# Kernel tuning notes

Hardware: AMD Instinct MI355X
Metric: run time of the kernel (lower is better)

Reference implementation:

```python
import math
import jax, jax.numpy as jnp
import numpy as np

NUM_HEADS = 8


def setup_inputs() -> dict:
    rng = jax.random.key(0)
    ks = jax.random.split(rng, 6)
    S, B, E = 2048, 4, 512
    scale = 1.0 / math.sqrt(E)  # xavier-ish init scale
    return {
        "query": jax.random.normal(ks[0], (S, B, E), jnp.float32),
        "key": jax.random.normal(ks[1], (S, B, E), jnp.float32),
        "value": jax.random.normal(ks[2], (S, B, E), jnp.float32),
        "attn_mask": jax.random.normal(ks[3], (B, S, S), jnp.float32),
        "in_proj_weight": jax.random.normal(ks[4], (3 * E, E), jnp.float32) * scale,
        "in_proj_bias": jnp.zeros((3 * E,), jnp.float32),
        "out_proj_weight": jax.random.normal(ks[5], (E, E), jnp.float32) * scale,
        "out_proj_bias": jnp.zeros((E,), jnp.float32),
    }


def reference(query, key, value, attn_mask, in_proj_weight, in_proj_bias,
              out_proj_weight, out_proj_bias):
    # Layout: [S, B, E] (batch_first=False)
    S, B, E = query.shape
    H = NUM_HEADS
    D = E // H
    w_q, w_k, w_v = jnp.split(in_proj_weight, 3, axis=0)  # each [E, E]
    b_q, b_k, b_v = jnp.split(in_proj_bias, 3)
    q = query @ w_q.T + b_q
    k = key @ w_k.T + b_k
    v = value @ w_v.T + b_v

    def to_heads(x):  # [S,B,E] -> [B,H,S,D]
        return x.reshape(S, B, H, D).transpose(1, 2, 0, 3)

    qh = to_heads(q) * (1.0 / math.sqrt(D))
    kh = to_heads(k)
    vh = to_heads(v)
    # full score matrix [B,H,S,S] with per-batch additive mask broadcast over heads
    scores = jnp.einsum('bhsd,bhtd->bhst', qh, kh) + attn_mask[:, None, :, :]
    attn = jax.nn.softmax(scores, axis=-1)
    out = jnp.einsum('bhst,bhtd->bhsd', attn, vh)
    out = out.transpose(2, 0, 1, 3).reshape(S, B, E)  # back to [S,B,E]
    return out @ out_proj_weight.T + out_proj_bias
```

## Files before the change

### kernel.cpp

```cpp
#include <hip/hip_runtime.h>


#define L2E 1.44269504088896340736f

typedef __attribute__((ext_vector_type(8))) __bf16 bf16x8;
typedef __attribute__((ext_vector_type(4))) float f32x4;

static __device__ __forceinline__ unsigned pk2(float a, float b) {
    union { unsigned u; __bf16 h[2]; } cv;
    cv.h[0] = (__bf16)a; cv.h[1] = (__bf16)b;
    return cv.u;
}

static __device__ __forceinline__ unsigned short f2bf(float f) {
    union { unsigned short s; __bf16 h; } cv;
    cv.h = (__bf16)f;
    return cv.s;
}

__global__ __launch_bounds__(256) void qkv_kernel(
    const float* __restrict__ Xq, const float* __restrict__ Xk,
    const float* __restrict__ Xv, const float* __restrict__ W,
    const float* __restrict__ bias,
    unsigned short* __restrict__ Qp, unsigned short* __restrict__ Kp,
    unsigned short* __restrict__ Vt)
{
    __shared__ unsigned short lA[128][40];
    __shared__ unsigned short lB[128][40];

    const int z = blockIdx.z;
    const float* X  = (z == 0) ? Xq : (z == 1) ? Xk : Xv;
    const float* Wz = W + (size_t)z * 512 * 512;
    const int rb = blockIdx.y * 128;
    const int nb = blockIdx.x * 128;
    const int tid  = threadIdx.x;
    const int lane = tid & 63, wave = tid >> 6;
    const int wr = wave >> 1, wc = wave & 1;
    const int lq = lane & 15, lg = lane >> 4;

    f32x4 acc[4][4];
#pragma unroll
    for (int i = 0; i < 4; ++i)
#pragma unroll
        for (int j = 0; j < 4; ++j) acc[i][j] = (f32x4){0.f, 0.f, 0.f, 0.f};

    const int srow = tid >> 1;
    const int scol = (tid & 1) * 16;

    for (int kt = 0; kt < 16; ++kt) {
        const int k0 = kt * 32;
        if (kt) __syncthreads();
        {
            const float* g = X + (size_t)(rb + srow) * 512 + k0 + scol;
            float4 x0 = *(const float4*)(g + 0);
            float4 x1 = *(const float4*)(g + 4);
            float4 x2 = *(const float4*)(g + 8);
            float4 x3 = *(const float4*)(g + 12);
            uint4 w0, w1;
            w0.x = pk2(x0.x, x0.y); w0.y = pk2(x0.z, x0.w);
            w0.z = pk2(x1.x, x1.y); w0.w = pk2(x1.z, x1.w);
            w1.x = pk2(x2.x, x2.y); w1.y = pk2(x2.z, x2.w);
            w1.z = pk2(x3.x, x3.y); w1.w = pk2(x3.z, x3.w);
            *(uint4*)&lA[srow][scol] = w0;
            *(uint4*)&lA[srow][scol + 8] = w1;
        }
        {
            const float* g = Wz + (size_t)(nb + srow) * 512 + k0 + scol;
            float4 x0 = *(const float4*)(g + 0);
            float4 x1 = *(const float4*)(g + 4);
            float4 x2 = *(const float4*)(g + 8);
            float4 x3 = *(const float4*)(g + 12);
            uint4 w0, w1;
            w0.x = pk2(x0.x, x0.y); w0.y = pk2(x0.z, x0.w);
            w0.z = pk2(x1.x, x1.y); w0.w = pk2(x1.z, x1.w);
            w1.x = pk2(x2.x, x2.y); w1.y = pk2(x2.z, x2.w);
            w1.z = pk2(x3.x, x3.y); w1.w = pk2(x3.z, x3.w);
            *(uint4*)&lB[srow][scol] = w0;
            *(uint4*)&lB[srow][scol + 8] = w1;
        }
        __syncthreads();

        bf16x8 af[4], bf[4];
#pragma unroll
        for (int mi = 0; mi < 4; ++mi)
            af[mi] = *(const bf16x8*)&lA[wr * 64 + mi * 16 + lq][lg * 8];
#pragma unroll
        for (int ni = 0; ni < 4; ++ni)
            bf[ni] = *(const bf16x8*)&lB[wc * 64 + ni * 16 + lq][lg * 8];
#pragma unroll
        for (int mi = 0; mi < 4; ++mi)
#pragma unroll
            for (int ni = 0; ni < 4; ++ni)
                acc[mi][ni] = __builtin_amdgcn_mfma_f32_16x16x32_bf16(
                    af[mi], bf[ni], acc[mi][ni], 0, 0, 0);
    }

    const float* bz = bias + z * 512;
#pragma unroll
    for (int ni = 0; ni < 4; ++ni) {
        const int n = nb + wc * 64 + ni * 16 + lq;
        const float bv = bz[n];
        const int h = n >> 6, d = n & 63;
#pragma unroll
        for (int mi = 0; mi < 4; ++mi) {
#pragma unroll
            for (int r = 0; r < 4; ++r) {
                const int t = rb + wr * 64 + mi * 16 + lg * 4 + r;
                float v = acc[mi][ni][r] + bv;
                const int s = t >> 2, b = t & 3;
                if (z == 0) {
                    v *= 0.125f * L2E;
                    Qp[((size_t)(b * 8 + h) * 2048 + s) * 64 + d] = f2bf(v);
                } else if (z == 1) {
                    Kp[((size_t)(b * 8 + h) * 2048 + s) * 64 + d] = f2bf(v);
                } else {
                    Vt[((size_t)(b * 8 + h) * 64 + d) * 2048 + s] = f2bf(v);
                }
            }
        }
    }
}

__global__ __launch_bounds__(256) void attn_kernel(
    const unsigned short* __restrict__ Qp, const unsigned short* __restrict__ Kp,
    const unsigned short* __restrict__ Vt, const float* __restrict__ mask,
    unsigned short* __restrict__ AO)
{
    __shared__ unsigned short lK[2][64][64];
    __shared__ unsigned short lV[2][64][64];
    __shared__ unsigned short lP[4][16][40];

    const int bh = blockIdx.y;
    const int b = bh >> 3, h = bh & 7;
    const int qb = blockIdx.x * 64;
    const int tid  = threadIdx.x;
    const int lane = tid & 63, wave = tid >> 6;
    const int lq = lane & 15, lg = lane >> 4;
    const int sw = lq & 7;

    const int qg = qb + wave * 16 + lq;
    const unsigned short* Kbase = Kp + (size_t)bh * 2048 * 64;
    const unsigned short* Vbase = Vt + (size_t)bh * 64 * 2048;
    const float* mrow = mask + ((size_t)b * 2048 + qg) * 2048 + lg * 4;

    const bf16x8 qf0 = *(const bf16x8*)(Qp + ((size_t)bh * 2048 + qg) * 64 + lg * 8);
    const bf16x8 qf1 = *(const bf16x8*)(Qp + ((size_t)bh * 2048 + qg) * 64 + 32 + lg * 8);

    f32x4 o[4];
#pragma unroll
    for (int di = 0; di < 4; ++di) o[di] = (f32x4){0.f, 0.f, 0.f, 0.f};
    float lsum = 0.f;

    const int srow = tid >> 2;
    const int scu  = (tid & 3) * 2;
    const int su0  = (scu    ) ^ (srow & 7);
    const int su1  = (scu + 1) ^ (srow & 7);
    const unsigned short* gK = Kbase + (size_t)srow * 64 + scu * 8;
    const unsigned short* gV = Vbase + (size_t)srow * 2048 + scu * 8;

    uint4 ka = *(const uint4*)(gK);
    uint4 kc = *(const uint4*)(gK + 8);
    uint4 va = *(const uint4*)(gV);
    uint4 vc = *(const uint4*)(gV + 8);
    float4 mv[4];
#pragma unroll
    for (int sub = 0; sub < 4; ++sub)
        mv[sub] = *(const float4*)(mrow + sub * 16);
    *(uint4*)&lK[0][srow][su0 * 8] = ka;
    *(uint4*)&lK[0][srow][su1 * 8] = kc;
    *(uint4*)&lV[0][srow][su0 * 8] = va;
    *(uint4*)&lV[0][srow][su1 * 8] = vc;
    __syncthreads();

    for (int kb = 0; kb < 32; ++kb) {
        const int cur = kb & 1;
        float4 mnx[4];
        if (kb < 31) {
            const size_t kv = (size_t)(kb + 1) * 64;
            ka = *(const uint4*)(gK + kv * 64);
            kc = *(const uint4*)(gK + kv * 64 + 8);
            va = *(const uint4*)(gV + kv);
            vc = *(const uint4*)(gV + kv + 8);
#pragma unroll
            for (int sub = 0; sub < 4; ++sub)
                mnx[sub] = *(const float4*)(mrow + kv + sub * 16);
        }

        f32x4 zv[4];
        __builtin_amdgcn_s_setprio(1);
#pragma unroll
        for (int sub = 0; sub < 4; ++sub) {
            bf16x8 a0 = *(const bf16x8*)&lK[cur][sub * 16 + lq][(lg ^ sw) * 8];
            bf16x8 a1 = *(const bf16x8*)&lK[cur][sub * 16 + lq][((4 | lg) ^ sw) * 8];
            f32x4 sf = (f32x4){mv[sub].x * L2E, mv[sub].y * L2E,
                               mv[sub].z * L2E, mv[sub].w * L2E};
            sf = __builtin_amdgcn_mfma_f32_16x16x32_bf16(a0, qf0, sf, 0, 0, 0);
            sf = __builtin_amdgcn_mfma_f32_16x16x32_bf16(a1, qf1, sf, 0, 0, 0);
            zv[sub] = sf;
        }
        __builtin_amdgcn_s_setprio(0);

#pragma unroll
        for (int ks = 0; ks < 2; ++ks) {
#pragma unroll
            for (int s2 = 0; s2 < 2; ++s2) {
                const int sub = ks * 2 + s2;
                float e0 = exp2f(zv[sub][0]);
                float e1 = exp2f(zv[sub][1]);
                float e2 = exp2f(zv[sub][2]);
                float e3 = exp2f(zv[sub][3]);
                lsum += (e0 + e1) + (e2 + e3);
                *(uint2*)&lP[wave][lq][s2 * 16 + lg * 4] =
                    make_uint2(pk2(e0, e1), pk2(e2, e3));
            }
            bf16x8 pb = *(const bf16x8*)&lP[wave][lq][lg * 8];
            __builtin_amdgcn_s_setprio(1);
#pragma unroll
            for (int di = 0; di < 4; ++di) {
                bf16x8 av = *(const bf16x8*)
                    &lV[cur][di * 16 + lq][(((ks * 4) | lg) ^ sw) * 8];
                o[di] = __builtin_amdgcn_mfma_f32_16x16x32_bf16(av, pb, o[di], 0, 0, 0);
            }
            __builtin_amdgcn_s_setprio(0);
        }

        if (kb < 31) {
            *(uint4*)&lK[cur ^ 1][srow][su0 * 8] = ka;
            *(uint4*)&lK[cur ^ 1][srow][su1 * 8] = kc;
            *(uint4*)&lV[cur ^ 1][srow][su0 * 8] = va;
            *(uint4*)&lV[cur ^ 1][srow][su1 * 8] = vc;
#pragma unroll
            for (int sub = 0; sub < 4; ++sub) mv[sub] = mnx[sub];
        }
        __syncthreads();
    }

    lsum += __shfl_xor(lsum, 16);
    lsum += __shfl_xor(lsum, 32);
    const float inv = 1.0f / lsum;

    unsigned short* aobase = AO + ((size_t)qg * 4 + b) * 512 + h * 64;
#pragma unroll
    for (int di = 0; di < 4; ++di) {
        const int d = di * 16 + lg * 4;
        *(uint2*)(aobase + d) = make_uint2(pk2(o[di][0] * inv, o[di][1] * inv),
                                           pk2(o[di][2] * inv, o[di][3] * inv));
    }
}

__global__ __launch_bounds__(256) void oproj_kernel(
    const unsigned short* __restrict__ A, const float* __restrict__ W,
    const float* __restrict__ bias, float* __restrict__ out)
{
    __shared__ unsigned short lA[128][40];
    __shared__ unsigned short lB[128][40];

    const int rb = blockIdx.y * 128;
    const int nb = blockIdx.x * 128;
    const int tid  = threadIdx.x;
    const int lane = tid & 63, wave = tid >> 6;
    const int wr = wave >> 1, wc = wave & 1;
    const int lq = lane & 15, lg = lane >> 4;

    f32x4 acc[4][4];
#pragma unroll
    for (int i = 0; i < 4; ++i)
#pragma unroll
        for (int j = 0; j < 4; ++j) acc[i][j] = (f32x4){0.f, 0.f, 0.f, 0.f};

    const int srow = tid >> 1;
    const int scol = (tid & 1) * 16;

    for (int kt = 0; kt < 16; ++kt) {
        const int k0 = kt * 32;
        if (kt) __syncthreads();
        {
            const unsigned short* g = A + (size_t)(rb + srow) * 512 + k0 + scol;
            *(uint4*)&lA[srow][scol]     = *(const uint4*)g;
            *(uint4*)&lA[srow][scol + 8] = *(const uint4*)(g + 8);
        }
        {
            const float* g = W + (size_t)(nb + srow) * 512 + k0 + scol;
            float4 x0 = *(const float4*)(g + 0);
            float4 x1 = *(const float4*)(g + 4);
            float4 x2 = *(const float4*)(g + 8);
            float4 x3 = *(const float4*)(g + 12);
            uint4 w0, w1;
            w0.x = pk2(x0.x, x0.y); w0.y = pk2(x0.z, x0.w);
            w0.z = pk2(x1.x, x1.y); w0.w = pk2(x1.z, x1.w);
            w1.x = pk2(x2.x, x2.y); w1.y = pk2(x2.z, x2.w);
            w1.z = pk2(x3.x, x3.y); w1.w = pk2(x3.z, x3.w);
            *(uint4*)&lB[srow][scol] = w0;
            *(uint4*)&lB[srow][scol + 8] = w1;
        }
        __syncthreads();

        bf16x8 af[4], bfr[4];
#pragma unroll
        for (int mi = 0; mi < 4; ++mi)
            af[mi] = *(const bf16x8*)&lA[wr * 64 + mi * 16 + lq][lg * 8];
#pragma unroll
        for (int ni = 0; ni < 4; ++ni)
            bfr[ni] = *(const bf16x8*)&lB[wc * 64 + ni * 16 + lq][lg * 8];
#pragma unroll
        for (int mi = 0; mi < 4; ++mi)
#pragma unroll
            for (int ni = 0; ni < 4; ++ni)
                acc[mi][ni] = __builtin_amdgcn_mfma_f32_16x16x32_bf16(
                    af[mi], bfr[ni], acc[mi][ni], 0, 0, 0);
    }

#pragma unroll
    for (int ni = 0; ni < 4; ++ni) {
        const int n = nb + wc * 64 + ni * 16 + lq;
        const float bv = bias[n];
#pragma unroll
        for (int mi = 0; mi < 4; ++mi) {
#pragma unroll
            for (int r = 0; r < 4; ++r) {
                const int t = rb + wr * 64 + mi * 16 + lg * 4 + r;
                out[(size_t)t * 512 + n] = acc[mi][ni][r] + bv;
            }
        }
    }
}

extern "C" void kernel_launch(void* const* d_in, const int* in_sizes, int n_in,
                              void* d_out, int out_size, void* d_ws, size_t ws_size,
                              hipStream_t stream)
{
    (void)in_sizes; (void)n_in; (void)out_size; (void)ws_size;
    const float* query = (const float*)d_in[0];
    const float* key   = (const float*)d_in[1];
    const float* value = (const float*)d_in[2];
    const float* mask  = (const float*)d_in[3];
    const float* w_in  = (const float*)d_in[4];
    const float* b_in  = (const float*)d_in[5];
    const float* w_out = (const float*)d_in[6];
    const float* b_out = (const float*)d_in[7];
    float* out = (float*)d_out;

    char* ws = (char*)d_ws;
    unsigned short* Qp = (unsigned short*)(ws);
    unsigned short* Kp = (unsigned short*)(ws + (size_t)8 * 1024 * 1024);
    unsigned short* Vt = (unsigned short*)(ws + (size_t)16 * 1024 * 1024);
    unsigned short* AO = (unsigned short*)(ws + (size_t)24 * 1024 * 1024);

    qkv_kernel<<<dim3(4, 64, 3), 256, 0, stream>>>(query, key, value, w_in, b_in,
                                                   Qp, Kp, Vt);
    attn_kernel<<<dim3(32, 32), 256, 0, stream>>>(Qp, Kp, Vt, mask, AO);
    oproj_kernel<<<dim3(4, 64), 256, 0, stream>>>(AO, w_out, b_out, out);
}
```

Before: 156.5 us.

## Switch attention to 32x32 MFMA with register-resident P via permlane swap

The attention kernel moves from 16x16x32 to 32x32x16 bf16 MFMA tiles, giving each wave 32 query rows and each block 128 queries, which halves the grid. The P matrix no longer goes through an LDS staging buffer: exp2 results are packed to bf16 and rearranged across lanes with v_permlane32_swap, then fed straight into the PV MFMA. The kv loop is unrolled by two with explicit ping-pong buffers and launch bounds request two blocks per CU. This cuts LDS traffic and synchronisation, but raises register pressure and leaves fewer blocks to spread across the CUs.

Result: no change. 157.6 us (+0.7%).

```diff
diff --git a/kernel.cpp b/kernel.cpp
--- a/kernel.cpp
+++ b/kernel.cpp
@@ -5,6 +5,7 @@
 
 typedef __attribute__((ext_vector_type(8))) __bf16 bf16x8;
 typedef __attribute__((ext_vector_type(4))) float f32x4;
+typedef __attribute__((ext_vector_type(16))) float f32x16;
 
 static __device__ __forceinline__ unsigned pk2(float a, float b) {
     union { unsigned u; __bf16 h[2]; } cv;
@@ -121,130 +122,186 @@
     }
 }
 
-__global__ __launch_bounds__(256) void attn_kernel(
+#define SWAP32(a, b) asm("v_permlane32_swap_b32 %0, %1" : "+v"(a), "+v"(b))
+
+#define COMPUTE(KBASE, VBASE, M) do {                                          \
+    bf16x8 pf[4];                                                              \
+    _Pragma("unroll")                                                          \
+    for (int kblk = 0; kblk < 2; ++kblk) {                                     \
+        f32x16 z;                                                              \
+        _Pragma("unroll")                                                      \
+        for (int g = 0; g < 4; ++g) {                                          \
+            z[4*g+0] = M[kblk][g].x * L2E;                                     \
+            z[4*g+1] = M[kblk][g].y * L2E;                                     \
+            z[4*g+2] = M[kblk][g].z * L2E;                                     \
+            z[4*g+3] = M[kblk][g].w * L2E;                                     \
+        }                                                                      \
+        __builtin_amdgcn_s_setprio(1);                                         \
+        _Pragma("unroll")                                                      \
+        for (int s = 0; s < 4; ++s) {                                          \
+            bf16x8 kf = *(const bf16x8*)((KBASE) + fof[kblk][s]);              \
+            z = __builtin_amdgcn_mfma_f32_32x32x16_bf16(kf, qf[s], z, 0,0,0);  \
+        }                                                                      \
+        __builtin_amdgcn_s_setprio(0);                                         \
+        float p[16];                                                           \
+        _Pragma("unroll")                                                      \
+        for (int i = 0; i < 16; ++i) p[i] = exp2f(z[i]);                       \
+        lsum += (((p[0]+p[1])+(p[2]+p[3])) + ((p[4]+p[5])+(p[6]+p[7])))        \
+              + (((p[8]+p[9])+(p[10]+p[11])) + ((p[12]+p[13])+(p[14]+p[15]))); \
+        unsigned a0 = pk2(p[0], p[1]),   b0 = pk2(p[4], p[5]);                 \
+        unsigned a1 = pk2(p[2], p[3]),   b1 = pk2(p[6], p[7]);                 \
+        SWAP32(a0, b0); SWAP32(a1, b1);                                        \
+        union { unsigned w[4]; bf16x8 v; } u0;                                 \
+        u0.w[0] = a0; u0.w[1] = a1; u0.w[2] = b0; u0.w[3] = b1;                \
+        pf[kblk*2] = u0.v;                                                     \
+        unsigned c0 = pk2(p[8], p[9]),   d0 = pk2(p[12], p[13]);               \
+        unsigned c1 = pk2(p[10], p[11]), d1 = pk2(p[14], p[15]);               \
+        SWAP32(c0, d0); SWAP32(c1, d1);                                        \
+        union { unsigned w[4]; bf16x8 v; } u1;                                 \
+        u1.w[0] = c0; u1.w[1] = c1; u1.w[2] = d0; u1.w[3] = d1;                \
+        pf[kblk*2+1] = u1.v;                                                   \
+    }                                                                          \
+    __builtin_amdgcn_s_setprio(1);                                             \
+    _Pragma("unroll")                                                          \
+    for (int s = 0; s < 4; ++s) {                                              \
+        bf16x8 vf0 = *(const bf16x8*)((VBASE) + fof[0][s]);                    \
+        o0 = __builtin_amdgcn_mfma_f32_32x32x16_bf16(vf0, pf[s], o0, 0,0,0);   \
+        bf16x8 vf1 = *(const bf16x8*)((VBASE) + fof[1][s]);                    \
+        o1 = __builtin_amdgcn_mfma_f32_32x32x16_bf16(vf1, pf[s], o1, 0,0,0);   \
+    }                                                                          \
+    __builtin_amdgcn_s_setprio(0);                                             \
+} while (0)
+
+__global__ __launch_bounds__(256, 2) void attn_kernel(
     const unsigned short* __restrict__ Qp, const unsigned short* __restrict__ Kp,
     const unsigned short* __restrict__ Vt, const float* __restrict__ mask,
     unsigned short* __restrict__ AO)
 {
     __shared__ unsigned short lK[2][64][64];
     __shared__ unsigned short lV[2][64][64];
-    __shared__ unsigned short lP[4][16][40];
 
     const int bh = blockIdx.y;
     const int b = bh >> 3, h = bh & 7;
-    const int qb = blockIdx.x * 64;
+    const int qb = blockIdx.x * 128;
     const int tid  = threadIdx.x;
     const int lane = tid & 63, wave = tid >> 6;
-    const int lq = lane & 15, lg = lane >> 4;
-    const int sw = lq & 7;
-
-    const int qg = qb + wave * 16 + lq;
-    const unsigned short* Kbase = Kp + (size_t)bh * 2048 * 64;
-    const unsigned short* Vbase = Vt + (size_t)bh * 64 * 2048;
-    const float* mrow = mask + ((size_t)b * 2048 + qg) * 2048 + lg * 4;
-
-    const bf16x8 qf0 = *(const bf16x8*)(Qp + ((size_t)bh * 2048 + qg) * 64 + lg * 8);
-    const bf16x8 qf1 = *(const bf16x8*)(Qp + ((size_t)bh * 2048 + qg) * 64 + 32 + lg * 8);
-
-    f32x4 o[4];
-#pragma unroll
-    for (int di = 0; di < 4; ++di) o[di] = (f32x4){0.f, 0.f, 0.f, 0.f};
+    const int lc = lane & 31, hi = lane >> 5;
+
+    const int qg = qb + wave * 32 + lc;
+
+    bf16x8 qf[4];
+    {
+        const unsigned short* qp = Qp + ((size_t)bh * 2048 + qg) * 64 + hi * 8;
+#pragma unroll
+        for (int s = 0; s < 4; ++s)
+            qf[s] = *(const bf16x8*)(qp + s * 16);
+    }
+
+    f32x16 o0, o1;
+#pragma unroll
+    for (int i = 0; i < 16; ++i) { o0[i] = 0.f; o1[i] = 0.f; }
     float lsum = 0.f;
+
+    int fof[2][4];
+#pragma unroll
+    for (int blk = 0; blk < 2; ++blk)
+#pragma unroll
+        for (int s = 0; s < 4; ++s)
+            fof[blk][s] = (blk * 32 + lc) * 128 +
+                          ((((s << 1) | hi) ^ (lane & 7)) * 16);
 
     const int srow = tid >> 2;
     const int scu  = (tid & 3) * 2;
     const int su0  = (scu    ) ^ (srow & 7);
     const int su1  = (scu + 1) ^ (srow & 7);
-    const unsigned short* gK = Kbase + (size_t)srow * 64 + scu * 8;
-    const unsigned short* gV = Vbase + (size_t)srow * 2048 + scu * 8;
-
-    uint4 ka = *(const uint4*)(gK);
-    uint4 kc = *(const uint4*)(gK + 8);
-    uint4 va = *(const uint4*)(gV);
-    uint4 vc = *(const uint4*)(gV + 8);
-    float4 mv[4];
-#pragma unroll
-    for (int sub = 0; sub < 4; ++sub)
-        mv[sub] = *(const float4*)(mrow + sub * 16);
-    *(uint4*)&lK[0][srow][su0 * 8] = ka;
-    *(uint4*)&lK[0][srow][su1 * 8] = kc;
-    *(uint4*)&lV[0][srow][su0 * 8] = va;
-    *(uint4*)&lV[0][srow][su1 * 8] = vc;
+    const unsigned short* gK = Kp + (size_t)bh * 2048 * 64 + (size_t)srow * 64 + scu * 8;
+    const unsigned short* gV = Vt + (size_t)bh * 64 * 2048 + (size_t)srow * 2048 + scu * 8;
+    const float* mbase = mask + ((size_t)b * 2048 + qg) * 2048 + hi * 4;
+
+    float4 mA[2][4], mB[2][4];
+
+    {
+        uint4 ka = *(const uint4*)(gK);
+        uint4 kc = *(const uint4*)(gK + 8);
+        uint4 va = *(const uint4*)(gV);
+        uint4 vc = *(const uint4*)(gV + 8);
+#pragma unroll
+        for (int kblk = 0; kblk < 2; ++kblk)
+#pragma unroll
+            for (int g = 0; g < 4; ++g)
+                mA[kblk][g] = *(const float4*)(mbase + kblk * 32 + g * 8);
+        *(uint4*)&lK[0][srow][su0 * 8] = ka;
+        *(uint4*)&lK[0][srow][su1 * 8] = kc;
+        *(uint4*)&lV[0][srow][su0 * 8] = va;
+        *(uint4*)&lV[0][srow][su1 * 8] = vc;
+    }
     __syncthreads();
 
-    for (int kb = 0; kb < 32; ++kb) {
-        const int cur = kb & 1;
-        float4 mnx[4];
-        if (kb < 31) {
-            const size_t kv = (size_t)(kb + 1) * 64;
-            ka = *(const uint4*)(gK + kv * 64);
-            kc = *(const uint4*)(gK + kv * 64 + 8);
-            va = *(const uint4*)(gV + kv);
-            vc = *(const uint4*)(gV + kv + 8);
-#pragma unroll
-            for (int sub = 0; sub < 4; ++sub)
-                mnx[sub] = *(const float4*)(mrow + kv + sub * 16);
-        }
-
-        f32x4 zv[4];
-        __builtin_amdgcn_s_setprio(1);
-#pragma unroll
-        for (int sub = 0; sub < 4; ++sub) {
-            bf16x8 a0 = *(const bf16x8*)&lK[cur][sub * 16 + lq][(lg ^ sw) * 8];
-            bf16x8 a1 = *(const bf16x8*)&lK[cur][sub * 16 + lq][((4 | lg) ^ sw) * 8];
-            f32x4 sf = (f32x4){mv[sub].x * L2E, mv[sub].y * L2E,
-                               mv[sub].z * L2E, mv[sub].w * L2E};
-            sf = __builtin_amdgcn_mfma_f32_16x16x32_bf16(a0, qf0, sf, 0, 0, 0);
-            sf = __builtin_amdgcn_mfma_f32_16x16x32_bf16(a1, qf1, sf, 0, 0, 0);
-            zv[sub] = sf;
-        }
-        __builtin_amdgcn_s_setprio(0);
-
-#pragma unroll
-        for (int ks = 0; ks < 2; ++ks) {
-#pragma unroll
-            for (int s2 = 0; s2 < 2; ++s2) {
-                const int sub = ks * 2 + s2;
-                float e0 = exp2f(zv[sub][0]);
-                float e1 = exp2f(zv[sub][1]);
-                float e2 = exp2f(zv[sub][2]);
-                float e3 = exp2f(zv[sub][3]);
-                lsum += (e0 + e1) + (e2 + e3);
-                *(uint2*)&lP[wave][lq][s2 * 16 + lg * 4] =
-                    make_uint2(pk2(e0, e1), pk2(e2, e3));
+    const unsigned short* pgK = gK + 64 * 64;
+    const unsigned short* pgV = gV + 64;
+    const float* pm = mbase + 64;
+
+    for (int kb2 = 0; kb2 < 16; ++kb2) {
+        {
+            uint4 ka = *(const uint4*)(pgK);
+            uint4 kc = *(const uint4*)(pgK + 8);
+            uint4 va = *(const uint4*)(pgV);
+            uint4 vc = *(const uint4*)(pgV + 8);
+#pragma unroll
+            for (int kblk = 0; kblk < 2; ++kblk)
+#pragma unroll
+                for (int g = 0; g < 4; ++g)
+                    mB[kblk][g] = *(const float4*)(pm + kblk * 32 + g * 8);
+            pgK += 64 * 64; pgV += 64; pm += 64;
+
+            COMPUTE((const char*)&lK[0][0][0], (const char*)&lV[0][0][0], mA);
+
+            *(uint4*)&lK[1][srow][su0 * 8] = ka;
+            *(uint4*)&lK[1][srow][su1 * 8] = kc;
+            *(uint4*)&lV[1][srow][su0 * 8] = va;
+            *(uint4*)&lV[1][srow][su1 * 8] = vc;
+            __syncthreads();
+        }
+        {
+            uint4 ka, kc, va, vc;
+            if (kb2 < 15) {
+                ka = *(const uint4*)(pgK);
+                kc = *(const uint4*)(pgK + 8);
+                va = *(const uint4*)(pgV);
+                vc = *(const uint4*)(pgV + 8);
+#pragma unroll
+                for (int kblk = 0; kblk < 2; ++kblk)
+#pragma unroll
+                    for (int g = 0; g < 4; ++g)
+                        mA[kblk][g] = *(const float4*)(pm + kblk * 32 + g * 8);
+                pgK += 64 * 64; pgV += 64; pm += 64;
             }
-            bf16x8 pb = *(const bf16x8*)&lP[wave][lq][lg * 8];
-            __builtin_amdgcn_s_setprio(1);
-#pragma unroll
-            for (int di = 0; di < 4; ++di) {
-                bf16x8 av = *(const bf16x8*)
-                    &lV[cur][di * 16 + lq][(((ks * 4) | lg) ^ sw) * 8];
-                o[di] = __builtin_amdgcn_mfma_f32_16x16x32_bf16(av, pb, o[di], 0, 0, 0);
+
+            COMPUTE((const char*)&lK[1][0][0], (const char*)&lV[1][0][0], mB);
+
+            if (kb2 < 15) {
+                *(uint4*)&lK[0][srow][su0 * 8] = ka;
+                *(uint4*)&lK[0][srow][su1 * 8] = kc;
+                *(uint4*)&lV[0][srow][su0 * 8] = va;
+                *(uint4*)&lV[0][srow][su1 * 8] = vc;
+                __syncthreads();
             }
-            __builtin_amdgcn_s_setprio(0);
-        }
-
-        if (kb < 31) {
-            *(uint4*)&lK[cur ^ 1][srow][su0 * 8] = ka;
-            *(uint4*)&lK[cur ^ 1][srow][su1 * 8] = kc;
-            *(uint4*)&lV[cur ^ 1][srow][su0 * 8] = va;
-            *(uint4*)&lV[cur ^ 1][srow][su1 * 8] = vc;
-#pragma unroll
-            for (int sub = 0; sub < 4; ++sub) mv[sub] = mnx[sub];
-        }
-        __syncthreads();
-    }
-
-    lsum += __shfl_xor(lsum, 16);
+        }
+    }
+
     lsum += __shfl_xor(lsum, 32);
     const float inv = 1.0f / lsum;
 
-    unsigned short* aobase = AO + ((size_t)qg * 4 + b) * 512 + h * 64;
-#pragma unroll
-    for (int di = 0; di < 4; ++di) {
-        const int d = di * 16 + lg * 4;
-        *(uint2*)(aobase + d) = make_uint2(pk2(o[di][0] * inv, o[di][1] * inv),
-                                           pk2(o[di][2] * inv, o[di][3] * inv));
+    unsigned short* ao = AO + ((size_t)qg * 4 + b) * 512 + h * 64;
+#pragma unroll
+    for (int g = 0; g < 4; ++g) {
+        const int d0 = g * 8 + hi * 4;
+        *(uint2*)(ao + d0) =
+            make_uint2(pk2(o0[4*g+0] * inv, o0[4*g+1] * inv),
+                       pk2(o0[4*g+2] * inv, o0[4*g+3] * inv));
+        *(uint2*)(ao + 32 + d0) =
+            make_uint2(pk2(o1[4*g+0] * inv, o1[4*g+1] * inv),
+                       pk2(o1[4*g+2] * inv, o1[4*g+3] * inv));
     }
 }
 
@@ -348,6 +405,6 @@
 
     qkv_kernel<<<dim3(4, 64, 3), 256, 0, stream>>>(query, key, value, w_in, b_in,
                                                    Qp, Kp, Vt);
-    attn_kernel<<<dim3(32, 32), 256, 0, stream>>>(Qp, Kp, Vt, mask, AO);
+    attn_kernel<<<dim3(16, 32), 256, 0, stream>>>(Qp, Kp, Vt, mask, AO);
     oproj_kernel<<<dim3(4, 64), 256, 0, stream>>>(AO, w_out, b_out, out);
 }
```
